# Kernel tuning notes

Measured on AMD Instinct MI355X. Metric: run time of the kernel, lower is better.

Reference implementation:

```python
import jax, jax.numpy as jnp
import numpy as np
import math

B, L, D, H, R = 2, 1024, 768, 12, 256
DH = D // H  # 64


def layernorm(x, g, b, eps=1e-5):
    mu = jnp.mean(x, axis=-1, keepdims=True)
    var = jnp.mean((x - mu) ** 2, axis=-1, keepdims=True)
    return (x - mu) / jnp.sqrt(var + eps) * g + b


def setup_inputs() -> dict:
    key = jax.random.key(0)
    ks = jax.random.split(key, 8)
    x = jax.random.normal(ks[0], (B, L, D), dtype=jnp.float32)
    conv_w = jax.random.normal(ks[1], (D, 3), dtype=jnp.float32) * 0.3   # depthwise k=3
    conv_b = jnp.zeros((D,), jnp.float32)
    ln_g = jnp.ones((D,), jnp.float32)
    ln_b = jnp.zeros((D,), jnp.float32)
    qkv_w = jax.random.normal(ks[2], (3 * D, D), dtype=jnp.float32) / math.sqrt(D)
    qkv_b = jnp.zeros((3 * D,), jnp.float32)
    bn_w1 = jax.random.normal(ks[3], (R, D), dtype=jnp.float32) / math.sqrt(D)
    bn_w2 = jax.random.normal(ks[4], (H * 5, R), dtype=jnp.float32) / math.sqrt(R)
    temperature = jnp.ones((1,), jnp.float32) * 0.5
    proj_w = jax.random.normal(ks[5], (D, D), dtype=jnp.float32) / math.sqrt(D)
    proj_b = jnp.zeros((D,), jnp.float32)
    mn_g = jnp.ones((DH,), jnp.float32)
    mn_b = jnp.zeros((DH,), jnp.float32)
    return {"x": x, "conv_w": conv_w, "conv_b": conv_b, "ln_g": ln_g, "ln_b": ln_b,
            "qkv_w": qkv_w, "qkv_b": qkv_b, "bn_w1": bn_w1, "bn_w2": bn_w2,
            "temperature": temperature, "proj_w": proj_w, "proj_b": proj_b,
            "mn_g": mn_g, "mn_b": mn_b}


def reference(x, conv_w, conv_b, ln_g, ln_b, qkv_w, qkv_b, bn_w1, bn_w2,
              temperature, proj_w, proj_b, mn_g, mn_b):
    Bx, Lx, Dx = x.shape
    # causal depthwise conv1d (kernel 3, pad 2 then drop last 2 == left-pad 2)
    xp = jnp.pad(x, ((0, 0), (2, 0), (0, 0)))
    conv = (xp[:, 0:Lx] * conv_w[:, 0] + xp[:, 1:Lx + 1] * conv_w[:, 1]
            + xp[:, 2:Lx + 2] * conv_w[:, 2]) + conv_b
    x_conv = x + conv
    xn = layernorm(x_conv, ln_g, ln_b)

    qkv = xn @ qkv_w.T + qkv_b
    q, k, v = jnp.split(qkv, 3, axis=-1)

    params = (jax.nn.silu(xn @ bn_w1.T) @ bn_w2.T).reshape(Bx, Lx, H, 5)
    sem_amp = jax.nn.sigmoid(params[..., 0])
    sem_phase = jnp.tanh(params[..., 1]) * math.pi
    ctx_amp = jax.nn.sigmoid(params[..., 2])
    ctx_phase = jnp.tanh(params[..., 3]) * math.pi
    decay = 0.3 + 0.65 * jax.nn.sigmoid(params[..., 4])  # (B,L,H)
    gate = jax.nn.sigmoid(sem_amp * ctx_amp * jnp.cos(sem_phase - ctx_phase) * temperature[0])

    q_f = (jax.nn.elu(q) + 1.0).reshape(Bx, Lx, H, DH)
    k_f = (jax.nn.elu(k) + 1.0).reshape(Bx, Lx, H, DH)
    v_f = v.reshape(Bx, Lx, H, DH)

    one_minus = 1.0 - decay                                    # (B,L,H)
    kv_input = jnp.einsum('blhd,blhe->blhde', k_f, v_f)        # (B,L,H,dh,dh)
    kv_input = jnp.clip(kv_input * (gate * one_minus)[..., None, None], -5.0, 5.0)

    df = jnp.exp(jnp.cumsum(jnp.log(decay), axis=1))           # (B,L,H)
    safe_df = df + 1e-8
    kv_states = jnp.cumsum(kv_input / safe_df[..., None, None], axis=1) * df[..., None, None]

    z = jnp.cumsum(k_f * one_minus[..., None] / safe_df[..., None], axis=1) * df[..., None]
    z = jnp.clip(z, -10000.0, 10000.0)

    out_num = jnp.einsum('blhd,blhde->blhe', q_f, kv_states)   # (B,L,H,dh)
    den = jnp.sum(q_f * z, axis=-1, keepdims=True) + 0.0001
    out = layernorm(out_num / den, mn_g, mn_b)                 # (B,L,H,dh)

    y = out.reshape(Bx, Lx, Dx) @ proj_w.T + proj_b
    return y, gate
```

## Files before the change

### kernel.cpp

```cpp
#include <hip/hip_runtime.h>
#include <math.h>

#define LL 1024
#define DD 768
#define HH 12
#define CL 16
#define NC 64
#define NBH 24

typedef __bf16 bf16x8 __attribute__((ext_vector_type(8)));
typedef __bf16 bf16x4 __attribute__((ext_vector_type(4)));
typedef float floatx4 __attribute__((ext_vector_type(4)));

typedef const void __attribute__((address_space(1)))* gas_ptr;
typedef void __attribute__((address_space(3)))* las_ptr;

__device__ __forceinline__ void gl_lds16(const void* g, void* s) {
  __builtin_amdgcn_global_load_lds((gas_ptr)g, (las_ptr)s, 16, 0, 0);
}

__device__ __forceinline__ float wave_sum64(float v) {
#pragma unroll
  for (int off = 32; off; off >>= 1) v += __shfl_xor(v, off, 64);
  return v;
}

__device__ __forceinline__ float sigm(float x) { return 1.0f / (1.0f + expf(-x)); }
__device__ __forceinline__ float clamp5(float x) {
  return __builtin_amdgcn_fmed3f(x, -5.f, 5.f);
}

__global__ __launch_bounds__(256) void prep_kernel(
    const float* __restrict__ x, const float* __restrict__ cw,
    const float* __restrict__ cb, const float* __restrict__ g,
    const float* __restrict__ bta, __bf16* __restrict__ xn,
    const float* __restrict__ qkvw, const float* __restrict__ bnw1,
    const float* __restrict__ projw, const float* __restrict__ w2,
    __bf16* __restrict__ wqb, __bf16* __restrict__ dp, __bf16* __restrict__ dw2) {
  if (blockIdx.x >= 2048) {
    int i = (blockIdx.x - 2048) * 256 + threadIdx.x;
    if (i >= 647168) return;
    bf16x4 o;
    if (i >= 638976) {
      int off = i - 638976;
      if (off < 3840) {
        float4 v = ((const float4*)w2)[off];
        o[0] = (__bf16)v.x; o[1] = (__bf16)v.y; o[2] = (__bf16)v.z; o[3] = (__bf16)v.w;
      } else {
        o[0] = (__bf16)0.f; o[1] = (__bf16)0.f; o[2] = (__bf16)0.f; o[3] = (__bf16)0.f;
      }
      ((bf16x4*)dw2)[off] = o;
      return;
    }
    const float* s; __bf16* d; int off, soff;
    if (i < 442368)      { s = qkvw;  d = wqb; off = i; soff = i; }
    else if (i < 491520) { s = bnw1;  d = wqb; off = i; soff = i - 442368; }
    else                 { s = projw; d = dp;  off = i - 491520; soff = off; }
    float4 v = ((const float4*)s)[soff];
    o[0] = (__bf16)v.x; o[1] = (__bf16)v.y; o[2] = (__bf16)v.z; o[3] = (__bf16)v.w;
    ((bf16x4*)d)[off] = o;
    return;
  }
  int row = blockIdx.x;
  int l = row & (LL - 1);
  const float* xr = x + (size_t)row * DD;
  __shared__ float red[16];
  float vals[3];
  float s = 0.f, ss = 0.f;
#pragma unroll
  for (int i = 0; i < 3; i++) {
    int d = threadIdx.x + i * 256;
    float x0 = xr[d];
    float xm1 = (l >= 1) ? xr[d - DD] : 0.f;
    float xm2 = (l >= 2) ? xr[d - 2 * DD] : 0.f;
    float c = xm2 * cw[d * 3 + 0] + xm1 * cw[d * 3 + 1] + x0 * cw[d * 3 + 2] + cb[d];
    float v = x0 + c;
    vals[i] = v; s += v; ss += v * v;
  }
  s = wave_sum64(s); ss = wave_sum64(ss);
  int wid = threadIdx.x >> 6;
  if ((threadIdx.x & 63) == 0) { red[wid * 2] = s; red[wid * 2 + 1] = ss; }
  __syncthreads();
  if (threadIdx.x == 0) {
    red[8] = red[0] + red[2] + red[4] + red[6];
    red[9] = red[1] + red[3] + red[5] + red[7];
  }
  __syncthreads();
  float mu = red[8] * (1.f / 768.f);
  float var = red[9] * (1.f / 768.f) - mu * mu;
  float inv = rsqrtf(var + 1e-5f);
  __bf16* xo = xn + (size_t)row * DD;
#pragma unroll
  for (int i = 0; i < 3; i++) {
    int d = threadIdx.x + i * 256;
    xo[d] = (__bf16)((vals[i] - mu) * inv * g[d] + bta[d]);
  }
}

template <int BM, int MODE, bool HASBIAS, bool OUTBF>
__global__ __launch_bounds__(256) void gemm_mfma_kernel(
    const __bf16* __restrict__ A, const __bf16* __restrict__ Bw,
    const float* __restrict__ bias, void* __restrict__ Cv, void* __restrict__ C2,
    int M, int N, int K) {
  constexpr int MI = BM / 32;
  __shared__ __attribute__((aligned(16))) __bf16 As[BM * 64];
  __shared__ __attribute__((aligned(16))) __bf16 Bs[128 * 64];
  int m0 = blockIdx.y * BM, n0 = blockIdx.x * 128;
  int tid = threadIdx.x;
  int w = tid >> 6, lane = tid & 63;
  int wm = w >> 1, wn = w & 1;
  int quad = lane >> 4, l16 = lane & 15;
  int lrow = lane >> 3;
  int lchunk = (lane & 7) ^ lrow;
  int R0 = w * 8;

  floatx4 acc[MI][4];
#pragma unroll
  for (int i = 0; i < MI; i++)
#pragma unroll
    for (int j = 0; j < 4; j++) acc[i][j] = (floatx4)0.f;

  for (int k0 = 0; k0 < K; k0 += 64) {
    __syncthreads();
#pragma unroll
    for (int r = 0; r < BM / 32; r++) {
      int row = r * 32 + R0 + lrow;
      gl_lds16(A + (size_t)(m0 + row) * K + k0 + lchunk * 8, &As[(r * 32 + R0) * 64]);
    }
#pragma unroll
    for (int r = 0; r < 4; r++) {
      int row = r * 32 + R0 + lrow;
      gl_lds16(Bw + (size_t)(n0 + row) * K + k0 + lchunk * 8, &Bs[(r * 32 + R0) * 64]);
    }
    __syncthreads();
#pragma unroll
    for (int s = 0; s < 2; s++) {
      bf16x8 af[MI], bfr[4];
      int csw = (s << 2) + quad;
#pragma unroll
      for (int i = 0; i < MI; i++) {
        int m = wm * (BM / 2) + i * 16 + l16;
        af[i] = *(const bf16x8*)&As[m * 64 + (csw ^ (l16 & 7)) * 8];
      }
#pragma unroll
      for (int j = 0; j < 4; j++) {
        int n = wn * 64 + j * 16 + l16;
        bfr[j] = *(const bf16x8*)&Bs[n * 64 + (csw ^ (l16 & 7)) * 8];
      }
#pragma unroll
      for (int i = 0; i < MI; i++)
#pragma unroll
        for (int j = 0; j < 4; j++)
          acc[i][j] = __builtin_amdgcn_mfma_f32_16x16x32_bf16(af[i], bfr[j], acc[i][j], 0, 0, 0);
    }
  }
#pragma unroll
  for (int j = 0; j < 4; j++) {
    int gcol = n0 + wn * 64 + j * 16 + l16;
    if (MODE == 3) {
      if (gcol < 2304) {
        float bv = bias[gcol];
        bool isqk = gcol < 1536;
#pragma unroll
        for (int i = 0; i < MI; i++) {
          int grow = m0 + wm * (BM / 2) + i * 16 + quad * 4;
#pragma unroll
          for (int r = 0; r < 4; r++) {
            float v = acc[i][j][r] + bv;
            if (isqk) v = (v > 0.f) ? v + 1.f : expf(v);
            ((__bf16*)Cv)[(size_t)(grow + r) * 2304 + gcol] = (__bf16)v;
          }
        }
      } else {
        int hcol = gcol - 2304;
#pragma unroll
        for (int i = 0; i < MI; i++) {
          int grow = m0 + wm * (BM / 2) + i * 16 + quad * 4;
#pragma unroll
          for (int r = 0; r < 4; r++) {
            float v = acc[i][j][r];
            v = v / (1.f + expf(-v));
            ((__bf16*)C2)[(size_t)(grow + r) * 256 + hcol] = (__bf16)v;
          }
        }
      }
    } else {
      float bv = HASBIAS ? bias[gcol] : 0.f;
#pragma unroll
      for (int i = 0; i < MI; i++) {
        int grow = m0 + wm * (BM / 2) + i * 16 + quad * 4;
#pragma unroll
        for (int r = 0; r < 4; r++) {
          float v = acc[i][j][r] + bv;
          if (OUTBF) ((__bf16*)Cv)[(size_t)(grow + r) * N + gcol] = (__bf16)v;
          else       ((float*)Cv)[(size_t)(grow + r) * N + gcol] = v;
        }
      }
    }
  }
}

__global__ __launch_bounds__(256) void params_df_kernel(
    const float* __restrict__ pp, const float* __restrict__ temp,
    float* __restrict__ gate, float* __restrict__ dec, float* __restrict__ dfb) {
  int bh = blockIdx.x;
  int b = bh / HH, h = bh - b * HH;
  int tid = threadIdx.x;
  int lane = tid & 63, wid = tid >> 6;
  float tv = temp[0];
  const float PI = 3.14159265358979323846f;
  double ls[4];
  double lsum = 0.0;
#pragma unroll
  for (int i = 0; i < 4; i++) {
    int l = tid * 4 + i;
    int row = (b << 10) + l;
    const float* p = pp + (size_t)row * 128 + h * 5;
    float p0 = p[0], p1 = p[1], p2 = p[2], p3 = p[3], p4 = p[4];
    float sa = sigm(p0);
    float sp = tanhf(p1) * PI;
    float ca = sigm(p2);
    float cp = tanhf(p3) * PI;
    float dc = 0.3f + 0.65f * sigm(p4);
    float gt = sigm(sa * ca * cosf(sp - cp) * tv);
    gate[row * HH + h] = gt;
    dec[(bh << 10) + l] = dc;
    lsum += (double)logf(dc);
    ls[i] = lsum;
  }
  double run = lsum;
#pragma unroll
  for (int off = 1; off < 64; off <<= 1) {
    double n = __shfl_up(run, off, 64);
    if (lane >= off) run += n;
  }
  __shared__ double wsum[4];
  if (lane == 63) wsum[wid] = run;
  __syncthreads();
  double wexcl = 0.0;
  for (int k = 0; k < wid; k++) wexcl += wsum[k];
  double excl = wexcl + run - lsum;
  float* dfo = dfb + (bh << 10) + tid * 4;
#pragma unroll
  for (int i = 0; i < 4; i++) dfo[i] = expf((float)(excl + ls[i]));
}

__global__ __launch_bounds__(256, 6) void scan_phase1(
    const __bf16* __restrict__ qkv, const float* __restrict__ dec,
    const float* __restrict__ df, const float* __restrict__ gate,
    __bf16* __restrict__ kvcs, float* __restrict__ zcs, float* __restrict__ Aarr,
    float* __restrict__ outp, float* __restrict__ zloc, float* __restrict__ pLoc) {
  int blk = blockIdx.x;
  int bh = blk >> 6, c = blk & (NC - 1);
  int b = bh / HH, h = bh - b * HH;
  int tid = threadIdx.x;
  int w = tid >> 6, e = tid & 63;
  int t0 = c * CL;
  __shared__ __attribute__((aligned(16))) __bf16 qbuf[CL][64];
  __shared__ __attribute__((aligned(16))) __bf16 kbuf[CL][64];
  __shared__ __attribute__((aligned(16))) __bf16 vbuf[CL][64];
  __shared__ float sbuf[CL][4];
  {
    int trow = ((w & 1) << 3) + (e >> 3);
    int chunk = e & 7;
    size_t rowbase = (size_t)(b * LL + t0 + trow) * 2304 + h * 64 + chunk * 8;
    if (w < 2) {
      gl_lds16(qkv + rowbase, &qbuf[(w & 1) << 3][0]);
      gl_lds16(qkv + rowbase + 768, &kbuf[(w & 1) << 3][0]);
    } else {
      gl_lds16(qkv + rowbase + 1536, &vbuf[(w & 1) << 3][0]);
    }
  }
  if (tid < CL) {
    int t = t0 + tid;
    float a = dec[bh * LL + t];
    float d = df[bh * LL + t];
    float r = d / (d + 1e-8f);
    float g = gate[(b * LL + t) * HH + h];
    sbuf[tid][0] = a; sbuf[tid][1] = r; sbuf[tid][2] = g * (1.f - a);
    sbuf[tid][3] = (1.f - a) * r;
  }
  __syncthreads();
  if (tid == 0) {
    float run = 1.f;
#pragma unroll
    for (int t = 0; t < CL; t++) { run *= sbuf[t][0]; pLoc[blk * 16 + t] = run; }
    Aarr[blk] = run;
  }
  float KV[16];
#pragma unroll
  for (int d = 0; d < 16; d++) KV[d] = 0.f;
  float z = 0.f;
  for (int t = 0; t < CL; t++) {
    float a = sbuf[t][0], r = sbuf[t][1], cs = sbuf[t][2], w1r = sbuf[t][3];
    float vc = (float)vbuf[t][e] * cs;
    float onp = 0.f;
    bf16x8 k0 = *(const bf16x8*)&kbuf[t][w << 4];
    bf16x8 k1 = *(const bf16x8*)&kbuf[t][(w << 4) + 8];
    bf16x8 q0 = *(const bf16x8*)&qbuf[t][w << 4];
    bf16x8 q1 = *(const bf16x8*)&qbuf[t][(w << 4) + 8];
#pragma unroll
    for (int j = 0; j < 8; j++) {
      float u = clamp5((float)k0[j] * vc);
      float nv = fmaf(a, KV[j], r * u);
      KV[j] = nv;
      onp = fmaf((float)q0[j], nv, onp);
    }
#pragma unroll
    for (int j = 0; j < 8; j++) {
      float u = clamp5((float)k1[j] * vc);
      float nv = fmaf(a, KV[8 + j], r * u);
      KV[8 + j] = nv;
      onp = fmaf((float)q1[j], nv, onp);
    }
    z = fmaf(a, z, (float)kbuf[t][e] * w1r);
    outp[(size_t)blk * 4096 + t * 256 + (w << 6) + e] = onp;
    if ((t >> 2) == w) zloc[(size_t)blk * 1024 + t * 64 + e] = z;
  }
  __bf16* kvo = kvcs + (size_t)blk * 4096 + (w << 4) * 64 + e;
#pragma unroll
  for (int d = 0; d < 16; d++) kvo[d * 64] = (__bf16)KV[d];
  if (w == 0) zcs[blk * 64 + e] = z;
}

__global__ __launch_bounds__(256) void combine_kernel(
    const float* __restrict__ Aarr, __bf16* __restrict__ kv, float* __restrict__ z) {
  int g = blockIdx.x * 256 + threadIdx.x;
  if (g < NBH * 4096) {
    int bh = g >> 12, idx = g & 4095;
    const float* Ap = Aarr + bh * NC;
    __bf16* p = kv + (size_t)bh * NC * 4096 + idx;
    float carry = 0.f;
#pragma unroll 8
    for (int c = 0; c < NC; c++) {
      float endv = (float)p[(size_t)c * 4096];
      p[(size_t)c * 4096] = (__bf16)carry;
      carry = fmaf(Ap[c], carry, endv);
    }
  } else {
    int g2 = g - NBH * 4096;
    if (g2 >= NBH * 64) return;
    int bh = g2 >> 6, idx = g2 & 63;
    const float* Ap = Aarr + bh * NC;
    float* p = z + bh * NC * 64 + idx;
    float carry = 0.f;
#pragma unroll 8
    for (int c = 0; c < NC; c++) {
      float endv = p[c * 64];
      p[c * 64] = carry;
      carry = fmaf(Ap[c], carry, endv);
    }
  }
}

__global__ __launch_bounds__(256) void scan_phase3(
    const __bf16* __restrict__ qkv, const __bf16* __restrict__ kvcs,
    const float* __restrict__ zcs, const float* __restrict__ outp,
    const float* __restrict__ zloc, const float* __restrict__ pLoc,
    const float* __restrict__ mng, const float* __restrict__ mnb,
    __bf16* __restrict__ att) {
  int blk = blockIdx.x;
  int bh = blk >> 6, c = blk & (NC - 1);
  int b = bh / HH, h = bh - b * HH;
  int tid = threadIdx.x;
  int w = tid >> 6, e = tid & 63;
  int t0 = c * CL;
  __shared__ __attribute__((aligned(16))) __bf16 qbuf[CL][64];
  __shared__ __attribute__((aligned(16))) __bf16 kvbuf[64][64];
  if (w < 2) {
    int trow = ((w & 1) << 3) + (e >> 3);
    int chunk = e & 7;
    gl_lds16(qkv + (size_t)(b * LL + t0 + trow) * 2304 + h * 64 + chunk * 8,
             &qbuf[(w & 1) << 3][0]);
  }
#pragma unroll
  for (int j = 0; j < 2; j++) {
    int m = (w << 1) | j;
    gl_lds16(kvcs + (size_t)blk * 4096 + m * 512 + e * 8, &kvbuf[m * 8][0]);
  }
  int t = tid >> 4;
  int e0 = (tid & 15) << 2;
  float P = pLoc[blk * 16 + t];
  float4 zi = *(const float4*)&zcs[blk * 64 + e0];
  float4 zl = *(const float4*)&zloc[(size_t)blk * 1024 + t * 64 + e0];
  float osum[4] = {0.f, 0.f, 0.f, 0.f};
#pragma unroll
  for (int ww = 0; ww < 4; ww++) {
    float4 o = *(const float4*)&outp[(size_t)blk * 4096 + t * 256 + ww * 64 + e0];
    osum[0] += o.x; osum[1] += o.y; osum[2] += o.z; osum[3] += o.w;
  }
  float4 mg = *(const float4*)&mng[e0];
  float4 mb = *(const float4*)&mnb[e0];
  __syncthreads();
  float ic[4] = {0.f, 0.f, 0.f, 0.f};
#pragma unroll
  for (int d0 = 0; d0 < 64; d0 += 8) {
    bf16x8 qv = *(const bf16x8*)&qbuf[t][d0];
#pragma unroll
    for (int j = 0; j < 8; j++) {
      bf16x4 kv = *(const bf16x4*)&kvbuf[d0 + j][e0];
      float qf = (float)qv[j];
#pragma unroll
      for (int x = 0; x < 4; x++) ic[x] = fmaf(qf, (float)kv[x], ic[x]);
    }
  }
  bf16x4 q4 = *(const bf16x4*)&qbuf[t][e0];
  float onum[4], zt[4];
  float s0 = 0.f, s1 = 0.f, s2 = 0.f;
  float zia[4] = {zi.x, zi.y, zi.z, zi.w};
  float zla[4] = {zl.x, zl.y, zl.z, zl.w};
#pragma unroll
  for (int x = 0; x < 4; x++) {
    onum[x] = fmaf(P, ic[x], osum[x]);
    float zv = fmaf(P, zia[x], zla[x]);
    zt[x] = __builtin_amdgcn_fmed3f(zv, -10000.f, 10000.f);
    s0 = fmaf((float)q4[x], zt[x], s0);
    s1 += onum[x];
    s2 = fmaf(onum[x], onum[x], s2);
  }
#pragma unroll
  for (int off = 1; off < 16; off <<= 1) {
    s0 += __shfl_xor(s0, off, 64);
    s1 += __shfl_xor(s1, off, 64);
    s2 += __shfl_xor(s2, off, 64);
  }
  float den = s0 + 1e-4f;
  float idn = 1.f / den;
  float mu = s1 * idn * (1.f / 64.f);
  float E2 = s2 * idn * idn * (1.f / 64.f);
  float var = E2 - mu * mu;
  float rst = rsqrtf(var + 1e-5f);
  float mga[4] = {mg.x, mg.y, mg.z, mg.w};
  float mba[4] = {mb.x, mb.y, mb.z, mb.w};
  bf16x4 ov;
#pragma unroll
  for (int x = 0; x < 4; x++) {
    float o = onum[x] * idn;
    ov[x] = (__bf16)((o - mu) * rst * mga[x] + mba[x]);
  }
  *(bf16x4*)&att[((size_t)(b * LL + t0 + t)) * DD + h * 64 + e0] = ov;
}

extern "C" void kernel_launch(void* const* d_in, const int* in_sizes, int n_in,
                              void* d_out, int out_size, void* d_ws, size_t ws_size,
                              hipStream_t stream) {
  (void)in_sizes; (void)n_in; (void)out_size; (void)ws_size;
  const float* x           = (const float*)d_in[0];
  const float* conv_w      = (const float*)d_in[1];
  const float* conv_b      = (const float*)d_in[2];
  const float* ln_g        = (const float*)d_in[3];
  const float* ln_b        = (const float*)d_in[4];
  const float* qkv_w       = (const float*)d_in[5];
  const float* qkv_b       = (const float*)d_in[6];
  const float* bn_w1       = (const float*)d_in[7];
  const float* bn_w2       = (const float*)d_in[8];
  const float* temperature = (const float*)d_in[9];
  const float* proj_w      = (const float*)d_in[10];
  const float* proj_b      = (const float*)d_in[11];
  const float* mn_g        = (const float*)d_in[12];
  const float* mn_b        = (const float*)d_in[13];

  float* y    = (float*)d_out;
  float* gate = y + 2 * 1024 * 768;

  char* ws = (char*)d_ws;
  __bf16* xn_bf   = (__bf16*)(ws);
  __bf16* att_bf  = xn_bf;
  __bf16* qkva    = (__bf16*)(ws + 3145728);
  __bf16* hbuf_bf = (__bf16*)(ws + 12582912);
  float*  pp      = (float*)(ws + 13631488);
  float*  dec     = (float*)(ws + 14680064);
  float*  dfb     = (float*)(ws + 14778368);
  __bf16* kvcs    = (__bf16*)(ws + 14876672);
  __bf16* wqb_bf  = (__bf16*)(ws + 14876672);
  float*  zcs     = (float*)(ws + 27459584);
  float*  Aarr    = (float*)(ws + 27852800);
  __bf16* projw_bf= (__bf16*)(ws + 27858944);
  __bf16* w2p_bf  = (__bf16*)(ws + 29038592);
  float*  outp    = (float*)(ws + 29104128);
  float*  zloc    = (float*)(ws + 54269952);
  float*  pLoc    = (float*)(ws + 60561408);

  prep_kernel<<<4576, 256, 0, stream>>>(x, conv_w, conv_b, ln_g, ln_b, xn_bf,
                                        qkv_w, bn_w1, proj_w, bn_w2,
                                        wqb_bf, projw_bf, w2p_bf);

  gemm_mfma_kernel<64, 3, true, false><<<dim3(20, 32), 256, 0, stream>>>(
      xn_bf, wqb_bf, qkv_b, qkva, hbuf_bf, 2048, 2560, 768);

  gemm_mfma_kernel<64, 0, false, false><<<dim3(1, 32), 256, 0, stream>>>(
      hbuf_bf, w2p_bf, nullptr, pp, nullptr, 2048, 128, 256);

  params_df_kernel<<<NBH, 256, 0, stream>>>(pp, temperature, gate, dec, dfb);

  scan_phase1<<<NBH * NC, 256, 0, stream>>>(qkva, dec, dfb, gate, kvcs, zcs, Aarr,
                                            outp, zloc, pLoc);

  combine_kernel<<<390, 256, 0, stream>>>(Aarr, kvcs, zcs);

  scan_phase3<<<NBH * NC, 256, 0, stream>>>(qkva, kvcs, zcs, outp, zloc, pLoc,
                                            mn_g, mn_b, att_bf);

  gemm_mfma_kernel<64, 0, true, false><<<dim3(6, 32), 256, 0, stream>>>(
      att_bf, projw_bf, proj_b, y, nullptr, 2048, 768, 768);
}
```

Baseline: 173.9 us.

## Fuse params projection, chunked scan and combine into one cooperative kernel

Replaces the small params GEMM, the params/decay kernel, scan phase 1, the combine kernel and scan phase 3 with a single cooperative kernel of 768 blocks that uses grid.sync between stages. The params projection is computed per chunk from hbuf in LDS with scalar FMAs, and the per-chunk log-decay prefix is computed in fp32 rather than double. The goal is to remove four kernel launches and their intermediate round trips. In exchange it adds grid-wide barriers, depends on 3 blocks per CU being resident, and gives up double-precision accumulation of the cumulative log-decay.

After: 173.4 us. No clear change (-0.3%).

```diff
diff --git a/kernel.cpp b/kernel.cpp
--- a/kernel.cpp
+++ b/kernel.cpp
@@ -1,5 +1,8 @@
 #include <hip/hip_runtime.h>
+#include <hip/hip_cooperative_groups.h>
 #include <math.h>
+
+namespace cg = cooperative_groups;
 
 #define LL 1024
 #define DD 768
@@ -200,6 +203,266 @@
   }
 }
 
+__global__ __launch_bounds__(256, 3) void scan_fused(
+    const __bf16* __restrict__ qkv, const __bf16* __restrict__ hbuf,
+    const float* __restrict__ w2, const float* __restrict__ temp,
+    __bf16* __restrict__ kvcs, float* __restrict__ zcs,
+    float* __restrict__ chLog, float* __restrict__ chA, float* __restrict__ chPre,
+    float* __restrict__ outp, float* __restrict__ zloc, float* __restrict__ pLoc,
+    const float* __restrict__ mng, const float* __restrict__ mnb,
+    float* __restrict__ gate, __bf16* __restrict__ att) {
+  cg::grid_group grid = cg::this_grid();
+  int tid = threadIdx.x;
+  int w = tid >> 6, e = tid & 63;
+
+  __shared__ __attribute__((aligned(16))) __bf16 qbuf[CL][64];
+  __shared__ __attribute__((aligned(16))) __bf16 kbuf[CL][64];
+  __shared__ __attribute__((aligned(16))) __bf16 vbuf[CL][64];
+  __shared__ __attribute__((aligned(16))) __bf16 hkv[64][64];
+  __shared__ float psb[CL][5];
+  __shared__ float decL[2][CL], gtL[2][CL], lpreL[2][CL];
+  __shared__ float sbuf[CL][4];
+
+#pragma unroll 1
+  for (int ci = 0; ci < 2; ci++) {
+    int gc = blockIdx.x + ci * 768;
+    int bh = gc >> 6, c = gc & (NC - 1);
+    int b = bh / HH, h = bh - b * HH;
+    int t0 = c * CL;
+    __syncthreads();
+    {
+      __bf16* h16 = &hkv[0][0];
+      int cc0 = (w << 6) + e;
+      gl_lds16(hbuf + (size_t)(b * LL + t0 + (cc0 >> 5)) * 256 + (cc0 & 31) * 8,
+               (char*)h16 + (w << 10));
+      int cc1 = 256 + cc0;
+      gl_lds16(hbuf + (size_t)(b * LL + t0 + (cc1 >> 5)) * 256 + (cc1 & 31) * 8,
+               (char*)h16 + 4096 + (w << 10));
+    }
+    __syncthreads();
+    if (tid < 80) {
+      int t = tid / 5, p = tid - t * 5;
+      const float* wr = w2 + (h * 5 + p) * 256;
+      const __bf16* hr = &hkv[0][0] + t * 256;
+      float acc = 0.f;
+#pragma unroll 8
+      for (int k = 0; k < 256; k++) acc = fmaf((float)hr[k], wr[k], acc);
+      psb[t][p] = acc;
+    }
+    __syncthreads();
+    if (tid < CL) {
+      int t = tid;
+      const float PI = 3.14159265358979323846f;
+      float sa = sigm(psb[t][0]), sp = tanhf(psb[t][1]) * PI;
+      float ca = sigm(psb[t][2]), cp = tanhf(psb[t][3]) * PI;
+      float dc = 0.3f + 0.65f * sigm(psb[t][4]);
+      float gt = sigm(sa * ca * cosf(sp - cp) * temp[0]);
+      gate[(size_t)(b * LL + t0 + t) * HH + h] = gt;
+      decL[ci][t] = dc;
+      gtL[ci][t] = gt;
+      lpreL[ci][t] = logf(dc);
+    }
+    __syncthreads();
+    if (tid == 0) {
+      float run = 0.f;
+#pragma unroll
+      for (int t = 0; t < CL; t++) { run += lpreL[ci][t]; lpreL[ci][t] = run; }
+      chLog[gc] = run;
+    }
+  }
+  grid.sync();
+
+  if (blockIdx.x < NBH && tid < 64) {
+    float v = chLog[blockIdx.x * 64 + tid];
+    float run = v;
+#pragma unroll
+    for (int off = 1; off < 64; off <<= 1) {
+      float n = __shfl_up(run, off, 64);
+      if (tid >= off) run += n;
+    }
+    chPre[blockIdx.x * 64 + tid] = run - v;
+    chA[blockIdx.x * 64 + tid] = expf(v);
+  }
+  grid.sync();
+
+#pragma unroll 1
+  for (int ci = 0; ci < 2; ci++) {
+    int gc = blockIdx.x + ci * 768;
+    int bh = gc >> 6, c = gc & (NC - 1);
+    int b = bh / HH, h = bh - b * HH;
+    int t0 = c * CL;
+    __syncthreads();
+    {
+      int trow = ((w & 1) << 3) + (e >> 3);
+      int chunk = e & 7;
+      size_t rowbase = (size_t)(b * LL + t0 + trow) * 2304 + h * 64 + chunk * 8;
+      if (w < 2) {
+        gl_lds16(qkv + rowbase, &qbuf[(w & 1) << 3][0]);
+        gl_lds16(qkv + rowbase + 768, &kbuf[(w & 1) << 3][0]);
+      } else {
+        gl_lds16(qkv + rowbase + 1536, &vbuf[(w & 1) << 3][0]);
+      }
+    }
+    if (tid < CL) {
+      int t = tid;
+      float base = chPre[gc];
+      float df = expf(base + lpreL[ci][t]);
+      float r = df / (df + 1e-8f);
+      float a = decL[ci][t];
+      float gt = gtL[ci][t];
+      sbuf[t][0] = a; sbuf[t][1] = r; sbuf[t][2] = gt * (1.f - a);
+      sbuf[t][3] = (1.f - a) * r;
+      pLoc[gc * 16 + t] = expf(lpreL[ci][t]);
+    }
+    __syncthreads();
+    float KV[16];
+#pragma unroll
+    for (int d = 0; d < 16; d++) KV[d] = 0.f;
+    float z = 0.f;
+    for (int t = 0; t < CL; t++) {
+      float a = sbuf[t][0], r = sbuf[t][1], cs = sbuf[t][2], w1r = sbuf[t][3];
+      float vc = (float)vbuf[t][e] * cs;
+      float onp = 0.f;
+      bf16x8 k0 = *(const bf16x8*)&kbuf[t][w << 4];
+      bf16x8 k1 = *(const bf16x8*)&kbuf[t][(w << 4) + 8];
+      bf16x8 q0 = *(const bf16x8*)&qbuf[t][w << 4];
+      bf16x8 q1 = *(const bf16x8*)&qbuf[t][(w << 4) + 8];
+#pragma unroll
+      for (int j = 0; j < 8; j++) {
+        float u = clamp5((float)k0[j] * vc);
+        float nv = fmaf(a, KV[j], r * u);
+        KV[j] = nv;
+        onp = fmaf((float)q0[j], nv, onp);
+      }
+#pragma unroll
+      for (int j = 0; j < 8; j++) {
+        float u = clamp5((float)k1[j] * vc);
+        float nv = fmaf(a, KV[8 + j], r * u);
+        KV[8 + j] = nv;
+        onp = fmaf((float)q1[j], nv, onp);
+      }
+      z = fmaf(a, z, (float)kbuf[t][e] * w1r);
+      outp[(size_t)gc * 4096 + t * 256 + (w << 6) + e] = onp;
+      if ((t >> 2) == w) zloc[(size_t)gc * 1024 + t * 64 + e] = z;
+    }
+    __bf16* kvo = kvcs + (size_t)gc * 4096 + (w << 4) * 64 + e;
+#pragma unroll
+    for (int d = 0; d < 16; d++) kvo[d * 64] = (__bf16)KV[d];
+    if (w == 0) zcs[gc * 64 + e] = z;
+  }
+  grid.sync();
+
+  {
+    int g = blockIdx.x * 256 + tid;
+    if (g < NBH * 4096) {
+      int cbh = g >> 12, idx = g & 4095;
+      const float* Ap = chA + cbh * NC;
+      __bf16* p = kvcs + (size_t)cbh * NC * 4096 + idx;
+      float carry = 0.f;
+#pragma unroll 8
+      for (int cc = 0; cc < NC; cc++) {
+        float endv = (float)p[(size_t)cc * 4096];
+        p[(size_t)cc * 4096] = (__bf16)carry;
+        carry = fmaf(Ap[cc], carry, endv);
+      }
+    } else if (g < NBH * 4096 + NBH * 64) {
+      int g2 = g - NBH * 4096;
+      int cbh = g2 >> 6, idx = g2 & 63;
+      const float* Ap = chA + cbh * NC;
+      float* p = zcs + cbh * NC * 64 + idx;
+      float carry = 0.f;
+#pragma unroll 8
+      for (int cc = 0; cc < NC; cc++) {
+        float endv = p[cc * 64];
+        p[cc * 64] = carry;
+        carry = fmaf(Ap[cc], carry, endv);
+      }
+    }
+  }
+  grid.sync();
+
+#pragma unroll 1
+  for (int ci = 0; ci < 2; ci++) {
+    int gc = blockIdx.x + ci * 768;
+    int bh = gc >> 6, c = gc & (NC - 1);
+    int b = bh / HH, h = bh - b * HH;
+    int t0 = c * CL;
+    __syncthreads();
+    if (w < 2) {
+      int trow = ((w & 1) << 3) + (e >> 3);
+      int chunk = e & 7;
+      gl_lds16(qkv + (size_t)(b * LL + t0 + trow) * 2304 + h * 64 + chunk * 8,
+               &qbuf[(w & 1) << 3][0]);
+    }
+#pragma unroll
+    for (int j = 0; j < 2; j++) {
+      int m = (w << 1) | j;
+      gl_lds16(kvcs + (size_t)gc * 4096 + m * 512 + e * 8, &hkv[m * 8][0]);
+    }
+    int t = tid >> 4;
+    int e0 = (tid & 15) << 2;
+    float P = pLoc[gc * 16 + t];
+    float4 zi = *(const float4*)&zcs[gc * 64 + e0];
+    float4 zl = *(const float4*)&zloc[(size_t)gc * 1024 + t * 64 + e0];
+    float osum[4] = {0.f, 0.f, 0.f, 0.f};
+#pragma unroll
+    for (int ww = 0; ww < 4; ww++) {
+      float4 o = *(const float4*)&outp[(size_t)gc * 4096 + t * 256 + ww * 64 + e0];
+      osum[0] += o.x; osum[1] += o.y; osum[2] += o.z; osum[3] += o.w;
+    }
+    float4 mg = *(const float4*)&mng[e0];
+    float4 mb = *(const float4*)&mnb[e0];
+    __syncthreads();
+    float ic[4] = {0.f, 0.f, 0.f, 0.f};
+#pragma unroll
+    for (int d0 = 0; d0 < 64; d0 += 8) {
+      bf16x8 qv = *(const bf16x8*)&qbuf[t][d0];
+#pragma unroll
+      for (int j = 0; j < 8; j++) {
+        bf16x4 kv = *(const bf16x4*)&hkv[d0 + j][e0];
+        float qf = (float)qv[j];
+#pragma unroll
+        for (int x = 0; x < 4; x++) ic[x] = fmaf(qf, (float)kv[x], ic[x]);
+      }
+    }
+    bf16x4 q4 = *(const bf16x4*)&qbuf[t][e0];
+    float onum[4], zt[4];
+    float s0 = 0.f, s1 = 0.f, s2 = 0.f;
+    float zia[4] = {zi.x, zi.y, zi.z, zi.w};
+    float zla[4] = {zl.x, zl.y, zl.z, zl.w};
+#pragma unroll
+    for (int x = 0; x < 4; x++) {
+      onum[x] = fmaf(P, ic[x], osum[x]);
+      float zv = fmaf(P, zia[x], zla[x]);
+      zt[x] = __builtin_amdgcn_fmed3f(zv, -10000.f, 10000.f);
+      s0 = fmaf((float)q4[x], zt[x], s0);
+      s1 += onum[x];
+      s2 = fmaf(onum[x], onum[x], s2);
+    }
+#pragma unroll
+    for (int off = 1; off < 16; off <<= 1) {
+      s0 += __shfl_xor(s0, off, 64);
+      s1 += __shfl_xor(s1, off, 64);
+      s2 += __shfl_xor(s2, off, 64);
+    }
+    float den = s0 + 1e-4f;
+    float idn = 1.f / den;
+    float mu = s1 * idn * (1.f / 64.f);
+    float E2 = s2 * idn * idn * (1.f / 64.f);
+    float var = E2 - mu * mu;
+    float rst = rsqrtf(var + 1e-5f);
+    float mga[4] = {mg.x, mg.y, mg.z, mg.w};
+    float mba[4] = {mb.x, mb.y, mb.z, mb.w};
+    bf16x4 ov;
+#pragma unroll
+    for (int x = 0; x < 4; x++) {
+      float o = onum[x] * idn;
+      ov[x] = (__bf16)((o - mu) * rst * mga[x] + mba[x]);
+    }
+    *(bf16x4*)&att[((size_t)(b * LL + t0 + t)) * DD + h * 64 + e0] = ov;
+  }
+}
+
 __global__ __launch_bounds__(256) void params_df_kernel(
     const float* __restrict__ pp, const float* __restrict__ temp,
     float* __restrict__ gate, float* __restrict__ dec, float* __restrict__ dfb) {
@@ -216,12 +479,11 @@
     int l = tid * 4 + i;
     int row = (b << 10) + l;
     const float* p = pp + (size_t)row * 128 + h * 5;
-    float p0 = p[0], p1 = p[1], p2 = p[2], p3 = p[3], p4 = p[4];
-    float sa = sigm(p0);
-    float sp = tanhf(p1) * PI;
-    float ca = sigm(p2);
-    float cp = tanhf(p3) * PI;
-    float dc = 0.3f + 0.65f * sigm(p4);
+    float sa = sigm(p[0]);
+    float sp = tanhf(p[1]) * PI;
+    float ca = sigm(p[2]);
+    float cp = tanhf(p[3]) * PI;
+    float dc = 0.3f + 0.65f * sigm(p[4]);
     float gt = sigm(sa * ca * cosf(sp - cp) * tv);
     gate[row * HH + h] = gt;
     dec[(bh << 10) + l] = dc;
@@ -480,6 +742,9 @@
   float*  outp    = (float*)(ws + 29104128);
   float*  zloc    = (float*)(ws + 54269952);
   float*  pLoc    = (float*)(ws + 60561408);
+  float*  chLog   = (float*)(ws + 60659712);
+  float*  chA     = (float*)(ws + 60665856);
+  float*  chPre   = (float*)(ws + 60672000);
 
   prep_kernel<<<4576, 256, 0, stream>>>(x, conv_w, conv_b, ln_g, ln_b, xn_bf,
                                         qkv_w, bn_w1, proj_w, bn_w2,
@@ -488,18 +753,29 @@
   gemm_mfma_kernel<64, 3, true, false><<<dim3(20, 32), 256, 0, stream>>>(
       xn_bf, wqb_bf, qkv_b, qkva, hbuf_bf, 2048, 2560, 768);
 
-  gemm_mfma_kernel<64, 0, false, false><<<dim3(1, 32), 256, 0, stream>>>(
-      hbuf_bf, w2p_bf, nullptr, pp, nullptr, 2048, 128, 256);
-
-  params_df_kernel<<<NBH, 256, 0, stream>>>(pp, temperature, gate, dec, dfb);
-
-  scan_phase1<<<NBH * NC, 256, 0, stream>>>(qkva, dec, dfb, gate, kvcs, zcs, Aarr,
-                                            outp, zloc, pLoc);
-
-  combine_kernel<<<390, 256, 0, stream>>>(Aarr, kvcs, zcs);
-
-  scan_phase3<<<NBH * NC, 256, 0, stream>>>(qkva, kvcs, zcs, outp, zloc, pLoc,
-                                            mn_g, mn_b, att_bf);
+  int coopBlocks = 0;
+  (void)hipOccupancyMaxActiveBlocksPerMultiprocessor(
+      &coopBlocks, reinterpret_cast<const void*>(scan_fused), 256, 0);
+
+  if (coopBlocks >= 3) {
+    void* kargs[] = {
+      (void*)&qkva, (void*)&hbuf_bf, (void*)&bn_w2, (void*)&temperature,
+      (void*)&kvcs, (void*)&zcs, (void*)&chLog, (void*)&chA, (void*)&chPre,
+      (void*)&outp, (void*)&zloc, (void*)&pLoc,
+      (void*)&mn_g, (void*)&mn_b, (void*)&gate, (void*)&att_bf
+    };
+    hipLaunchCooperativeKernel(reinterpret_cast<void*>(scan_fused),
+                               dim3(768), dim3(256), kargs, 0, stream);
+  } else {
+    gemm_mfma_kernel<64, 0, false, false><<<dim3(1, 32), 256, 0, stream>>>(
+        hbuf_bf, w2p_bf, nullptr, pp, nullptr, 2048, 128, 256);
+    params_df_kernel<<<NBH, 256, 0, stream>>>(pp, temperature, gate, dec, dfb);
+    scan_phase1<<<NBH * NC, 256, 0, stream>>>(qkva, dec, dfb, gate, kvcs, zcs,
+                                              Aarr, outp, zloc, pLoc);
+    combine_kernel<<<390, 256, 0, stream>>>(Aarr, kvcs, zcs);
+    scan_phase3<<<NBH * NC, 256, 0, stream>>>(qkva, kvcs, zcs, outp, zloc, pLoc,
+                                              mn_g, mn_b, att_bf);
+  }
 
   gemm_mfma_kernel<64, 0, true, false><<<dim3(6, 32), 256, 0, stream>>>(
       att_bf, projw_bf, proj_b, y, nullptr, 2048, 768, 768);
```
